# Optimization experiments

Measured on AMD Instinct MI355X. Metric: run time of the kernel, lower is better.

Reference implementation:

```python
import jax, jax.numpy as jnp
import numpy as np

SPARSITY = 0.8
LOCAL_WINDOW = 64


def setup_inputs() -> dict:
    key = jax.random.key(0)
    k1, k2 = jax.random.split(key)
    B, H, S = 2, 8, 2048
    attention_scores = jax.random.normal(k1, (B, H, S, S), dtype=jnp.float32)
    rand_u = jax.random.uniform(k2, (B, H, S, S), dtype=jnp.float32)
    return {"attention_scores": attention_scores, "rand_u": rand_u}


def reference(attention_scores, rand_u):
    B, H, S, _ = attention_scores.shape
    dt = attention_scores.dtype
    half = LOCAL_WINDOW // 2
    k = max(1, int(S * (1.0 - SPARSITY)))

    idx = jnp.arange(S)
    # local window mask: row i covers columns [max(0,i-half), min(S,i+half))
    local = ((idx[None, :] >= idx[:, None] - half) & (idx[None, :] < idx[:, None] + half)).astype(dt)  # (S,S)

    # global mask: topk over head-averaged importance, shared across heads
    importance = attention_scores.mean(axis=1)  # (B,S,S)
    _, top_g = jax.lax.top_k(importance, k)  # (B,S,k)
    gmask = jnp.zeros((B, S, S), dtype=dt).at[
        jnp.arange(B)[:, None, None], jnp.arange(S)[None, :, None], top_g
    ].set(1.0)

    # random sparsification mask
    random_mask = (rand_u < (1.0 - SPARSITY)).astype(dt)

    combined = ((local[None, None, :, :] + gmask[:, None, :, :] + random_mask) > 0).astype(dt)

    # sparsity enforcement: per-row topk of masked scores -> binary mask
    masked = attention_scores * combined
    _, top_f = jax.lax.top_k(masked, k)  # (B,H,S,k)
    final = jnp.zeros((B, H, S, S), dtype=dt).at[
        jnp.arange(B)[:, None, None, None],
        jnp.arange(H)[None, :, None, None],
        jnp.arange(S)[None, None, :, None],
        top_f,
    ].set(1.0)
    return final
```

## Files before the change

kernel.cpp:

```cpp
#include <hip/hip_runtime.h>
#include <cstdint>
#include <cstddef>

#define S_LEN   2048
#define N_HEADS 8
#define N_BATCH 2
#define TOPK    409
#define HALF_WIN 32
#define NT      256
#define PT      8
#define KEY_P0  0x80000000u
#define KEY_N0  0x7FFFFFFFu

__device__ __forceinline__ unsigned mono(float f) {
  unsigned u = __float_as_uint(f);
  return (u & 0x80000000u) ? ~u : (u | 0x80000000u);
}

__device__ __forceinline__ unsigned mbcnt64(unsigned long long m) {
  return __builtin_amdgcn_mbcnt_hi((unsigned)(m >> 32),
         __builtin_amdgcn_mbcnt_lo((unsigned)m, 0u));
}


struct SelScratch {
  unsigned hist[256];
  unsigned sbuf[256];
  unsigned bk[2];
};

__device__ __forceinline__ unsigned block_sum(unsigned c, SelScratch* s) {
  const int t = threadIdx.x;
  s->sbuf[t] = c;
  __syncthreads();
  #pragma unroll
  for (int d = 128; d > 0; d >>= 1) {
    if (t < d) s->sbuf[t] += s->sbuf[t + d];
    __syncthreads();
  }
  unsigned r = s->sbuf[0];
  __syncthreads();
  return r;
}

__device__ void radix_select(const unsigned* keys, int k, unsigned n0, unsigned n1,
                             SelScratch* s, unsigned* T_out, int* kk_out) {
  const int t = threadIdx.x;
  unsigned prefix = 0, done = 0;
  unsigned kk = (unsigned)k;
  #pragma unroll
  for (int shift = 24; shift >= 0; shift -= 8) {
    s->hist[t] = 0;
    __syncthreads();
    if (t == 0 && n0 != 0 && (KEY_P0 & done) == prefix)
      atomicAdd(&s->hist[(KEY_P0 >> shift) & 255u], n0);
    if (t == 1 && n1 != 0 && (KEY_N0 & done) == prefix)
      atomicAdd(&s->hist[(KEY_N0 >> shift) & 255u], n1);
    #pragma unroll
    for (int q = 0; q < PT; ++q) {
      unsigned kj = keys[t + NT * q];
      if (kj != KEY_P0 && kj != KEY_N0 && (kj & done) == prefix)
        atomicAdd(&s->hist[(kj >> shift) & 255u], 1u);
    }
    __syncthreads();
    s->sbuf[t] = s->hist[t];
    __syncthreads();
    for (int d = 1; d < 256; d <<= 1) {
      unsigned a = (t + d < 256) ? s->sbuf[t + d] : 0u;
      __syncthreads();
      s->sbuf[t] += a;
      __syncthreads();
    }
    unsigned suf_ge = s->sbuf[t];
    unsigned suf_gt = (t < 255) ? s->sbuf[t + 1] : 0u;
    if (suf_gt < kk && kk <= suf_ge) {
      s->bk[0] = (unsigned)t;
      s->bk[1] = kk - suf_gt;
    }
    __syncthreads();
    prefix |= s->bk[0] << shift;
    kk = s->bk[1];
    done |= 0xFFu << shift;
    __syncthreads();
  }
  *T_out = prefix;
  *kk_out = (int)kk;
}

__device__ __forceinline__ int stable_rank_base(int c, SelScratch* s) {
  const int t = threadIdx.x;
  s->sbuf[t] = (unsigned)c;
  __syncthreads();
  for (int d = 1; d < 256; d <<= 1) {
    unsigned a = (t >= d) ? s->sbuf[t - d] : 0u;
    __syncthreads();
    s->sbuf[t] += a;
    __syncthreads();
  }
  int base = (t == 0) ? 0 : (int)s->sbuf[t - 1];
  __syncthreads();
  return base;
}

__global__ __launch_bounds__(NT) void k_gmask(const float* __restrict__ scores,
                                              unsigned* __restrict__ gwords) {
  __shared__ __align__(16) unsigned keys[S_LEN];
  __shared__ SelScratch scr;
  __shared__ __align__(4) unsigned char gb[NT];
  const int t = threadIdx.x;
  const int blk = blockIdx.x;
  const int b = blk >> 11;
  const int i = blk & 2047;
  const size_t base = (((size_t)b * N_HEADS) * S_LEN + i) * S_LEN;

  unsigned c0 = 0, c1 = 0;
  #pragma unroll
  for (int s4 = 0; s4 < 2; ++s4) {
    const int j0 = (t + NT * s4) * 4;
    float4 a = *(const float4*)(scores + base + j0);
    #pragma unroll
    for (int h = 1; h < N_HEADS; ++h) {
      float4 x = *(const float4*)(scores + base + (size_t)h * S_LEN * S_LEN + j0);
      a.x += x.x; a.y += x.y; a.z += x.z; a.w += x.w;
    }
    unsigned kqa[4] __attribute__((aligned(16)));
    kqa[0] = mono(a.x); kqa[1] = mono(a.y); kqa[2] = mono(a.z); kqa[3] = mono(a.w);
    #pragma unroll
    for (int q = 0; q < 4; ++q) {
      c0 += (kqa[q] == KEY_P0);
      c1 += (kqa[q] == KEY_N0);
    }
    *(uint4*)(&keys[j0]) = *(uint4*)kqa;
  }
  __syncthreads();

  unsigned ns = block_sum(c0 | (c1 << 16), &scr);
  unsigned T; int kk;
  radix_select(keys, TOPK, ns & 0xFFFFu, ns >> 16, &scr, &T, &kk);

  int c = 0;
  #pragma unroll
  for (int e = 0; e < PT; ++e) c += (keys[t * PT + e] == T);
  int r = stable_rank_base(c, &scr);

  unsigned byte = 0;
  #pragma unroll
  for (int e = 0; e < PT; ++e) {
    unsigned kj = keys[t * PT + e];
    bool sel;
    if (kj > T)       sel = true;
    else if (kj == T) { sel = (r < kk); ++r; }
    else              sel = false;
    byte |= (unsigned)sel << e;
  }
  gb[t] = (unsigned char)byte;
  __syncthreads();
  if (t < 64) {
    unsigned wv = ((const unsigned*)gb)[t];
    int s0 = i - HALF_WIN - 32 * t;
    int e0 = i + HALF_WIN - 32 * t;
    s0 = s0 < 0 ? 0 : (s0 > 32 ? 32 : s0);
    e0 = e0 < 0 ? 0 : (e0 > 32 ? 32 : e0);
    unsigned lm = 0;
    if (e0 > s0) {
      unsigned hiM = (e0 == 32) ? 0xFFFFFFFFu : ((1u << e0) - 1u);
      lm = hiM & ~((1u << s0) - 1u);
    }
    gwords[(size_t)blk * 64 + t] = wv | lm;
  }
}


__device__ __forceinline__ void radix_range(const unsigned (&keys)[32], unsigned kk0,
                                            bool pos, unsigned* h, int l,
                                            unsigned& T_ret, unsigned& kk_ret) {
  unsigned prefix = 0, done = 0, kk = kk0;
  unsigned T = 0;
  bool resolved = false;
  #pragma unroll
  for (int pass = 0; pass < 4; ++pass) {
    const int shift = 24 - 8 * pass;
    *(uint4*)&h[l * 4] = make_uint4(0, 0, 0, 0);
    __threadfence_block();
    #pragma unroll
    for (int q = 0; q < 32; ++q) {
      unsigned kj = keys[q];
      bool in = pos ? (kj > KEY_P0) : (kj < KEY_N0);
      if (in && (kj & done) == prefix)
        atomicAdd(&h[(kj >> shift) & 255u], 1u);
    }
    __threadfence_block();
    uint4 hv = *(const uint4*)&h[l * 4];
    unsigned s3 = hv.w;
    unsigned s2 = hv.z + s3;
    unsigned s1 = hv.y + s2;
    unsigned s0 = hv.x + s1;
    unsigned inc = s0;
    #pragma unroll
    for (int d = 1; d < 64; d <<= 1) {
      unsigned o = __shfl_down(inc, d);
      inc += (l + d < 64) ? o : 0u;
    }
    const unsigned tail = inc - s0;
    const unsigned ge[4] = {s0 + tail, s1 + tail, s2 + tail, s3 + tail};
    const unsigned gt[4] = {s1 + tail, s2 + tail, s3 + tail, tail};
    unsigned packed = 0;
    bool found = false;
    #pragma unroll
    for (int q = 0; q < 4; ++q) {
      if (gt[q] < kk && kk <= ge[q]) {
        packed = ((unsigned)(4 * l + q) << 24) | ((ge[q] - gt[q]) << 12) | (kk - gt[q]);
        found = true;
      }
    }
    unsigned long long bal = __ballot(found);
    int srcl = __ffsll((long long)bal) - 1;
    packed = __shfl(packed, srcl);
    const unsigned cnt = (packed >> 12) & 0xFFFu;
    kk = packed & 0xFFFu;
    prefix |= (packed >> 24) << shift;
    done |= 0xFFu << shift;
    if (cnt == 1u) {
      unsigned cand = 0;
      #pragma unroll
      for (int q = 0; q < 32; ++q) {
        unsigned kj = keys[q];
        bool in = pos ? (kj > KEY_P0) : (kj < KEY_N0);
        if (in && (kj & done) == prefix) cand = kj;
      }
      #pragma unroll
      for (int d = 1; d < 64; d <<= 1) cand |= __shfl_xor(cand, d);
      T = cand;
      resolved = true;
      break;
    }
  }
  if (!resolved) T = prefix;
  T_ret = T;
  kk_ret = kk;
}

__global__ __launch_bounds__(256) void k_final(const float* __restrict__ scores,
                                               const float* __restrict__ randu,
                                               const unsigned* __restrict__ gwords,
                                               float* __restrict__ out) {
  __shared__ __align__(16) unsigned hist[4][256];
  __shared__ unsigned gm[4][64];
  const int l = threadIdx.x & 63;
  const int w = threadIdx.x >> 6;
  const int row = blockIdx.x * 4 + w;
  const int i = row & 2047;
  const int b = row >> 14;
  const size_t base = (size_t)row * S_LEN;
  const float thr = (float)(1.0 - 0.8);
  unsigned* h = hist[w];
  unsigned* g = gm[w];

  g[l] = gwords[((size_t)(b << 11) + i) * 64 + l];

  const int bitbase = 4 * (l & 7);
  unsigned keys[32];
  unsigned np = 0, n0 = 0, n1 = 0;
  #pragma unroll
  for (int s = 0; s < 8; ++s) {
    const int j0 = 256 * s + 4 * l;
    float4 sc = *(const float4*)(scores + base + j0);
    float4 ru = *(const float4*)(randu + base + j0);
    const unsigned gmw = g[8 * s + (l >> 3)];
    const float scv[4] = {sc.x, sc.y, sc.z, sc.w};
    const float ruv[4] = {ru.x, ru.y, ru.z, ru.w};
    #pragma unroll
    for (int e = 0; e < 4; ++e) {
      const unsigned u = __float_as_uint(scv[e]);
      const unsigned m = (unsigned)((int)u >> 31) | 0x80000000u;
      const bool comb = (((gmw >> (bitbase + e)) & 1u) != 0u) | (ruv[e] < thr);
      const unsigned key = (comb ? u : (u & 0x80000000u)) ^ m;
      keys[4 * s + e] = key;
      np += (unsigned)__popcll(__ballot(key > KEY_P0));
      n0 += (unsigned)__popcll(__ballot(key == KEY_P0));
      n1 += (unsigned)__popcll(__ballot(key == KEY_N0));
    }
  }

  unsigned T, kk;
  if (TOPK <= np) {
    radix_range(keys, TOPK, true, h, l, T, kk);
  } else if (TOPK <= np + n0) {
    T = KEY_P0; kk = TOPK - np;
  } else if (TOPK <= np + n0 + n1) {
    T = KEY_N0; kk = TOPK - np - n0;
  } else {
    radix_range(keys, TOPK - np - n0 - n1, false, h, l, T, kk);
  }

  unsigned S_tot = 0;
  #pragma unroll
  for (int s = 0; s < 8; ++s) {
    unsigned long long beq[4];
    unsigned pe[4];
    #pragma unroll
    for (int e = 0; e < 4; ++e) {
      beq[e] = __ballot(keys[4 * s + e] == T);
      pe[e] = (unsigned)__popcll(beq[e]);
    }
    const unsigned th = pe[0] + pe[1] + pe[2] + pe[3];
    float v[4] __attribute__((aligned(16)));
    if (S_tot + th <= kk) {
      #pragma unroll
      for (int e = 0; e < 4; ++e)
        v[e] = (keys[4 * s + e] >= T) ? 1.0f : 0.0f;
    } else if (S_tot >= kk) {
      #pragma unroll
      for (int e = 0; e < 4; ++e)
        v[e] = (keys[4 * s + e] > T) ? 1.0f : 0.0f;
    } else {
      unsigned mb[4], own[4];
      #pragma unroll
      for (int e = 0; e < 4; ++e) {
        mb[e]  = mbcnt64(beq[e]);
        own[e] = (unsigned)((beq[e] >> l) & 1ull);
      }
      const unsigned cross = S_tot + mb[0] + mb[1] + mb[2] + mb[3];
      unsigned run = 0;
      #pragma unroll
      for (int e = 0; e < 4; ++e) {
        unsigned kj = keys[4 * s + e];
        bool sel = (kj > T) || (kj == T && (cross + run) < kk);
        run += own[e];
        v[e] = sel ? 1.0f : 0.0f;
      }
    }
    S_tot += th;
    *(float4*)(out + base + 256 * s + 4 * l) = *(const float4*)v;
  }
}

extern "C" void kernel_launch(void* const* d_in, const int* in_sizes, int n_in,
                              void* d_out, int out_size, void* d_ws, size_t ws_size,
                              hipStream_t stream) {
  const float* scores = (const float*)d_in[0];
  const float* randu  = (const float*)d_in[1];
  float* out = (float*)d_out;
  unsigned* gwords = (unsigned*)d_ws;
  k_gmask<<<N_BATCH * S_LEN, NT, 0, stream>>>(scores, gwords);
  k_final<<<N_BATCH * N_HEADS * S_LEN / 4, 256, 0, stream>>>(scores, randu, gwords, out);
}
```

Baseline: 224.5 us.

## Fuse global-mask and final top-k into one kernel staging all heads in LDS

Merges the two kernels into one block per (batch,row) that loads all eight heads' score rows into shared memory. Warp 0 computes the head-averaged top-k global mask from LDS, then every warp does its per-head top-k. This removes the second full read of the scores tensor and the workspace round trip. It adds a fast path when the threshold key is unique. The cost is heavy LDS use, which can limit occupancy, and a serial phase in which the other waves idle while warp 0 computes the global mask.

```diff
diff --git a/kernel.cpp b/kernel.cpp
--- a/kernel.cpp
+++ b/kernel.cpp
@@ -7,176 +7,22 @@
 #define N_BATCH 2
 #define TOPK    409
 #define HALF_WIN 32
-#define NT      256
-#define PT      8
 #define KEY_P0  0x80000000u
 #define KEY_N0  0x7FFFFFFFu
-
-__device__ __forceinline__ unsigned mono(float f) {
-  unsigned u = __float_as_uint(f);
-  return (u & 0x80000000u) ? ~u : (u | 0x80000000u);
-}
 
 __device__ __forceinline__ unsigned mbcnt64(unsigned long long m) {
   return __builtin_amdgcn_mbcnt_hi((unsigned)(m >> 32),
          __builtin_amdgcn_mbcnt_lo((unsigned)m, 0u));
 }
 
-
-struct SelScratch {
-  unsigned hist[256];
-  unsigned sbuf[256];
-  unsigned bk[2];
-};
-
-__device__ __forceinline__ unsigned block_sum(unsigned c, SelScratch* s) {
-  const int t = threadIdx.x;
-  s->sbuf[t] = c;
-  __syncthreads();
-  #pragma unroll
-  for (int d = 128; d > 0; d >>= 1) {
-    if (t < d) s->sbuf[t] += s->sbuf[t + d];
-    __syncthreads();
-  }
-  unsigned r = s->sbuf[0];
-  __syncthreads();
-  return r;
-}
-
-__device__ void radix_select(const unsigned* keys, int k, unsigned n0, unsigned n1,
-                             SelScratch* s, unsigned* T_out, int* kk_out) {
-  const int t = threadIdx.x;
-  unsigned prefix = 0, done = 0;
-  unsigned kk = (unsigned)k;
-  #pragma unroll
-  for (int shift = 24; shift >= 0; shift -= 8) {
-    s->hist[t] = 0;
-    __syncthreads();
-    if (t == 0 && n0 != 0 && (KEY_P0 & done) == prefix)
-      atomicAdd(&s->hist[(KEY_P0 >> shift) & 255u], n0);
-    if (t == 1 && n1 != 0 && (KEY_N0 & done) == prefix)
-      atomicAdd(&s->hist[(KEY_N0 >> shift) & 255u], n1);
-    #pragma unroll
-    for (int q = 0; q < PT; ++q) {
-      unsigned kj = keys[t + NT * q];
-      if (kj != KEY_P0 && kj != KEY_N0 && (kj & done) == prefix)
-        atomicAdd(&s->hist[(kj >> shift) & 255u], 1u);
-    }
-    __syncthreads();
-    s->sbuf[t] = s->hist[t];
-    __syncthreads();
-    for (int d = 1; d < 256; d <<= 1) {
-      unsigned a = (t + d < 256) ? s->sbuf[t + d] : 0u;
-      __syncthreads();
-      s->sbuf[t] += a;
-      __syncthreads();
-    }
-    unsigned suf_ge = s->sbuf[t];
-    unsigned suf_gt = (t < 255) ? s->sbuf[t + 1] : 0u;
-    if (suf_gt < kk && kk <= suf_ge) {
-      s->bk[0] = (unsigned)t;
-      s->bk[1] = kk - suf_gt;
-    }
-    __syncthreads();
-    prefix |= s->bk[0] << shift;
-    kk = s->bk[1];
-    done |= 0xFFu << shift;
-    __syncthreads();
-  }
-  *T_out = prefix;
-  *kk_out = (int)kk;
-}
-
-__device__ __forceinline__ int stable_rank_base(int c, SelScratch* s) {
-  const int t = threadIdx.x;
-  s->sbuf[t] = (unsigned)c;
-  __syncthreads();
-  for (int d = 1; d < 256; d <<= 1) {
-    unsigned a = (t >= d) ? s->sbuf[t - d] : 0u;
-    __syncthreads();
-    s->sbuf[t] += a;
-    __syncthreads();
-  }
-  int base = (t == 0) ? 0 : (int)s->sbuf[t - 1];
-  __syncthreads();
-  return base;
-}
-
-__global__ __launch_bounds__(NT) void k_gmask(const float* __restrict__ scores,
-                                              unsigned* __restrict__ gwords) {
-  __shared__ __align__(16) unsigned keys[S_LEN];
-  __shared__ SelScratch scr;
-  __shared__ __align__(4) unsigned char gb[NT];
-  const int t = threadIdx.x;
-  const int blk = blockIdx.x;
-  const int b = blk >> 11;
-  const int i = blk & 2047;
-  const size_t base = (((size_t)b * N_HEADS) * S_LEN + i) * S_LEN;
-
-  unsigned c0 = 0, c1 = 0;
-  #pragma unroll
-  for (int s4 = 0; s4 < 2; ++s4) {
-    const int j0 = (t + NT * s4) * 4;
-    float4 a = *(const float4*)(scores + base + j0);
-    #pragma unroll
-    for (int h = 1; h < N_HEADS; ++h) {
-      float4 x = *(const float4*)(scores + base + (size_t)h * S_LEN * S_LEN + j0);
-      a.x += x.x; a.y += x.y; a.z += x.z; a.w += x.w;
-    }
-    unsigned kqa[4] __attribute__((aligned(16)));
-    kqa[0] = mono(a.x); kqa[1] = mono(a.y); kqa[2] = mono(a.z); kqa[3] = mono(a.w);
-    #pragma unroll
-    for (int q = 0; q < 4; ++q) {
-      c0 += (kqa[q] == KEY_P0);
-      c1 += (kqa[q] == KEY_N0);
-    }
-    *(uint4*)(&keys[j0]) = *(uint4*)kqa;
-  }
-  __syncthreads();
-
-  unsigned ns = block_sum(c0 | (c1 << 16), &scr);
-  unsigned T; int kk;
-  radix_select(keys, TOPK, ns & 0xFFFFu, ns >> 16, &scr, &T, &kk);
-
-  int c = 0;
-  #pragma unroll
-  for (int e = 0; e < PT; ++e) c += (keys[t * PT + e] == T);
-  int r = stable_rank_base(c, &scr);
-
-  unsigned byte = 0;
-  #pragma unroll
-  for (int e = 0; e < PT; ++e) {
-    unsigned kj = keys[t * PT + e];
-    bool sel;
-    if (kj > T)       sel = true;
-    else if (kj == T) { sel = (r < kk); ++r; }
-    else              sel = false;
-    byte |= (unsigned)sel << e;
-  }
-  gb[t] = (unsigned char)byte;
-  __syncthreads();
-  if (t < 64) {
-    unsigned wv = ((const unsigned*)gb)[t];
-    int s0 = i - HALF_WIN - 32 * t;
-    int e0 = i + HALF_WIN - 32 * t;
-    s0 = s0 < 0 ? 0 : (s0 > 32 ? 32 : s0);
-    e0 = e0 < 0 ? 0 : (e0 > 32 ? 32 : e0);
-    unsigned lm = 0;
-    if (e0 > s0) {
-      unsigned hiM = (e0 == 32) ? 0xFFFFFFFFu : ((1u << e0) - 1u);
-      lm = hiM & ~((1u << s0) - 1u);
-    }
-    gwords[(size_t)blk * 64 + t] = wv | lm;
-  }
-}
-
-
 __device__ __forceinline__ void radix_range(const unsigned (&keys)[32], unsigned kk0,
                                             bool pos, unsigned* h, int l,
-                                            unsigned& T_ret, unsigned& kk_ret) {
+                                            unsigned& T_ret, unsigned& kk_ret,
+                                            bool& cnt1) {
   unsigned prefix = 0, done = 0, kk = kk0;
   unsigned T = 0;
   bool resolved = false;
+  cnt1 = false;
   #pragma unroll
   for (int pass = 0; pass < 4; ++pass) {
     const int shift = 24 - 8 * pass;
@@ -232,6 +78,7 @@
       for (int d = 1; d < 64; d <<= 1) cand |= __shfl_xor(cand, d);
       T = cand;
       resolved = true;
+      cnt1 = true;
       break;
     }
   }
@@ -240,59 +87,38 @@
   kk_ret = kk;
 }
 
-__global__ __launch_bounds__(256) void k_final(const float* __restrict__ scores,
-                                               const float* __restrict__ randu,
-                                               const unsigned* __restrict__ gwords,
-                                               float* __restrict__ out) {
-  __shared__ __align__(16) unsigned hist[4][256];
-  __shared__ unsigned gm[4][64];
-  const int l = threadIdx.x & 63;
-  const int w = threadIdx.x >> 6;
-  const int row = blockIdx.x * 4 + w;
-  const int i = row & 2047;
-  const int b = row >> 14;
-  const size_t base = (size_t)row * S_LEN;
-  const float thr = (float)(1.0 - 0.8);
-  unsigned* h = hist[w];
-  unsigned* g = gm[w];
-
-  g[l] = gwords[((size_t)(b << 11) + i) * 64 + l];
-
-  const int bitbase = 4 * (l & 7);
-  unsigned keys[32];
-  unsigned np = 0, n0 = 0, n1 = 0;
-  #pragma unroll
-  for (int s = 0; s < 8; ++s) {
-    const int j0 = 256 * s + 4 * l;
-    float4 sc = *(const float4*)(scores + base + j0);
-    float4 ru = *(const float4*)(randu + base + j0);
-    const unsigned gmw = g[8 * s + (l >> 3)];
-    const float scv[4] = {sc.x, sc.y, sc.z, sc.w};
-    const float ruv[4] = {ru.x, ru.y, ru.z, ru.w};
-    #pragma unroll
-    for (int e = 0; e < 4; ++e) {
-      const unsigned u = __float_as_uint(scv[e]);
-      const unsigned m = (unsigned)((int)u >> 31) | 0x80000000u;
-      const bool comb = (((gmw >> (bitbase + e)) & 1u) != 0u) | (ruv[e] < thr);
-      const unsigned key = (comb ? u : (u & 0x80000000u)) ^ m;
-      keys[4 * s + e] = key;
-      np += (unsigned)__popcll(__ballot(key > KEY_P0));
-      n0 += (unsigned)__popcll(__ballot(key == KEY_P0));
-      n1 += (unsigned)__popcll(__ballot(key == KEY_N0));
-    }
-  }
-
-  unsigned T, kk;
+__device__ __forceinline__ void resolve_T(const unsigned (&keys)[32], unsigned* h,
+                                          int l, unsigned& T, unsigned& kk,
+                                          bool& cnt1) {
+  unsigned np = 0;
+  #pragma unroll
+  for (int q = 0; q < 32; ++q)
+    np += (unsigned)__popcll(__ballot(keys[q] > KEY_P0));
   if (TOPK <= np) {
-    radix_range(keys, TOPK, true, h, l, T, kk);
-  } else if (TOPK <= np + n0) {
-    T = KEY_P0; kk = TOPK - np;
-  } else if (TOPK <= np + n0 + n1) {
-    T = KEY_N0; kk = TOPK - np - n0;
+    radix_range(keys, TOPK, true, h, l, T, kk, cnt1);
   } else {
-    radix_range(keys, TOPK - np - n0 - n1, false, h, l, T, kk);
-  }
-
+    unsigned n0 = 0, n1 = 0;
+    #pragma unroll
+    for (int q = 0; q < 32; ++q) {
+      n0 += (unsigned)__popcll(__ballot(keys[q] == KEY_P0));
+      n1 += (unsigned)__popcll(__ballot(keys[q] == KEY_N0));
+    }
+    if (TOPK <= np + n0)           { T = KEY_P0; kk = TOPK - np;      cnt1 = (n0 == 1); }
+    else if (TOPK <= np + n0 + n1) { T = KEY_N0; kk = TOPK - np - n0; cnt1 = (n1 == 1); }
+    else radix_range(keys, TOPK - np - n0 - n1, false, h, l, T, kk, cnt1);
+  }
+}
+
+__device__ __forceinline__ unsigned select_bits(const unsigned (&keys)[32],
+                                                unsigned T, unsigned kk,
+                                                bool cnt1, int l) {
+  unsigned bits = 0;
+  if (cnt1) {
+    #pragma unroll
+    for (int q = 0; q < 32; ++q)
+      bits |= (keys[q] >= T ? 1u : 0u) << q;
+    return bits;
+  }
   unsigned S_tot = 0;
   #pragma unroll
   for (int s = 0; s < 8; ++s) {
@@ -304,15 +130,14 @@
       pe[e] = (unsigned)__popcll(beq[e]);
     }
     const unsigned th = pe[0] + pe[1] + pe[2] + pe[3];
-    float v[4] __attribute__((aligned(16)));
     if (S_tot + th <= kk) {
       #pragma unroll
       for (int e = 0; e < 4; ++e)
-        v[e] = (keys[4 * s + e] >= T) ? 1.0f : 0.0f;
+        bits |= (keys[4 * s + e] >= T ? 1u : 0u) << (4 * s + e);
     } else if (S_tot >= kk) {
       #pragma unroll
       for (int e = 0; e < 4; ++e)
-        v[e] = (keys[4 * s + e] > T) ? 1.0f : 0.0f;
+        bits |= (keys[4 * s + e] > T ? 1u : 0u) << (4 * s + e);
     } else {
       unsigned mb[4], own[4];
       #pragma unroll
@@ -327,11 +152,101 @@
         unsigned kj = keys[4 * s + e];
         bool sel = (kj > T) || (kj == T && (cross + run) < kk);
         run += own[e];
-        v[e] = sel ? 1.0f : 0.0f;
+        bits |= (sel ? 1u : 0u) << (4 * s + e);
       }
     }
     S_tot += th;
-    *(float4*)(out + base + 256 * s + 4 * l) = *(const float4*)v;
+  }
+  return bits;
+}
+
+__global__ __launch_bounds__(512, 4) void k_fused(const float* __restrict__ scores,
+                                                  const float* __restrict__ randu,
+                                                  float* __restrict__ out) {
+  __shared__ __align__(16) float sc_lds[N_HEADS][S_LEN];
+  __shared__ __align__(16) unsigned hist[N_HEADS][256];
+  __shared__ unsigned char gbytes[512];
+  const int l = threadIdx.x & 63;
+  const int w = threadIdx.x >> 6;
+  const int bi = blockIdx.x;
+  const int b = bi >> 11;
+  const int i = bi & 2047;
+  const size_t row = (((size_t)(b * N_HEADS + w)) * S_LEN + i) * S_LEN;
+  const float thr = (float)(1.0 - 0.8);
+
+  unsigned rndbits = 0;
+  #pragma unroll
+  for (int s = 0; s < 8; ++s) {
+    const int j0 = 256 * s + 4 * l;
+    float4 sc = *(const float4*)(scores + row + j0);
+    float4 ru = *(const float4*)(randu + row + j0);
+    *(float4*)&sc_lds[w][j0] = sc;
+    rndbits |= (ru.x < thr ? 1u : 0u) << (4 * s + 0);
+    rndbits |= (ru.y < thr ? 1u : 0u) << (4 * s + 1);
+    rndbits |= (ru.z < thr ? 1u : 0u) << (4 * s + 2);
+    rndbits |= (ru.w < thr ? 1u : 0u) << (4 * s + 3);
+  }
+  __syncthreads();
+
+  if (w == 0) {
+    unsigned gkeys[32];
+    #pragma unroll
+    for (int s = 0; s < 8; ++s) {
+      const int j0 = 256 * s + 4 * l;
+      float4 a = *(const float4*)&sc_lds[0][j0];
+      #pragma unroll
+      for (int hh = 1; hh < N_HEADS; ++hh) {
+        float4 x = *(const float4*)&sc_lds[hh][j0];
+        a.x += x.x; a.y += x.y; a.z += x.z; a.w += x.w;
+      }
+      const float av[4] = {a.x, a.y, a.z, a.w};
+      #pragma unroll
+      for (int e = 0; e < 4; ++e) {
+        unsigned u = __float_as_uint(av[e]);
+        gkeys[4 * s + e] = (u & 0x80000000u) ? ~u : (u | 0x80000000u);
+      }
+    }
+    unsigned T, kk; bool cnt1;
+    resolve_T(gkeys, hist[0], l, T, kk, cnt1);
+    unsigned bits = select_bits(gkeys, T, kk, cnt1, l);
+    const int lo = i - HALF_WIN;
+    #pragma unroll
+    for (int s = 0; s < 8; ++s) {
+      const int j0 = 256 * s + 4 * l;
+      unsigned nib = (bits >> (4 * s)) & 0xFu;
+      #pragma unroll
+      for (int e = 0; e < 4; ++e)
+        nib |= ((unsigned)(j0 + e - lo) < 64u ? 1u : 0u) << e;
+      gbytes[64 * s + l] = (unsigned char)nib;
+    }
+  }
+  __syncthreads();
+
+  unsigned keys[32];
+  #pragma unroll
+  for (int s = 0; s < 8; ++s) {
+    const int j0 = 256 * s + 4 * l;
+    float4 sc = *(const float4*)&sc_lds[w][j0];
+    const unsigned cn = (unsigned)gbytes[64 * s + l] | ((rndbits >> (4 * s)) & 0xFu);
+    const float scv[4] = {sc.x, sc.y, sc.z, sc.w};
+    #pragma unroll
+    for (int e = 0; e < 4; ++e) {
+      const unsigned u = __float_as_uint(scv[e]);
+      const unsigned m = (unsigned)((int)u >> 31) | 0x80000000u;
+      const bool comb = ((cn >> e) & 1u) != 0u;
+      keys[4 * s + e] = (comb ? u : (u & 0x80000000u)) ^ m;
+    }
+  }
+  unsigned T, kk; bool cnt1;
+  resolve_T(keys, hist[w], l, T, kk, cnt1);
+  unsigned bits = select_bits(keys, T, kk, cnt1, l);
+  #pragma unroll
+  for (int s = 0; s < 8; ++s) {
+    float v[4] __attribute__((aligned(16)));
+    #pragma unroll
+    for (int e = 0; e < 4; ++e)
+      v[e] = ((bits >> (4 * s + e)) & 1u) ? 1.0f : 0.0f;
+    *(float4*)(out + row + 256 * s + 4 * l) = *(const float4*)v;
   }
 }
 
@@ -341,7 +256,6 @@
   const float* scores = (const float*)d_in[0];
   const float* randu  = (const float*)d_in[1];
   float* out = (float*)d_out;
-  unsigned* gwords = (unsigned*)d_ws;
-  k_gmask<<<N_BATCH * S_LEN, NT, 0, stream>>>(scores, gwords);
-  k_final<<<N_BATCH * N_HEADS * S_LEN / 4, 256, 0, stream>>>(scores, randu, gwords, out);
-}
+  (void)d_ws; (void)ws_size;
+  k_fused<<<N_BATCH * S_LEN, 512, 0, stream>>>(scores, randu, out);
+}
```

Measured after the change: 210.2 us. 6.4% less time.
